# Kernel optimization log

Hardware: AMD Instinct MI355X
Metric: run time of the kernel (lower is better)

## Reference

```python
import jax, jax.numpy as jnp
import numpy as np

N_HEADS = 8

def setup_inputs() -> dict:
    key = jax.random.key(0)
    ks = jax.random.split(key, 7)
    B, S, D = 4, 2048, 512
    s = 1.0 / np.sqrt(D)
    return {
        "input_Q": jax.random.normal(ks[0], (B, S, D), jnp.float32),
        "input_K": jax.random.normal(ks[1], (B, S, D), jnp.float32),
        "input_V": jax.random.normal(ks[2], (B, S, D), jnp.float32),
        "W_Q": jax.random.normal(ks[3], (D, D), jnp.float32) * s,
        "W_K": jax.random.normal(ks[4], (D, D), jnp.float32) * s,
        "W_V": jax.random.normal(ks[5], (D, D), jnp.float32) * s,
        "W_O": jax.random.normal(ks[6], (D, D), jnp.float32) * s,
    }

def reference(input_Q, input_K, input_V, W_Q, W_K, W_V, W_O):
    B, Sq, D = input_Q.shape
    Sk = input_K.shape[1]
    H = N_HEADS
    d_k = D // H
    # torch nn.Linear(bias=False): y = x @ W.T
    def proj(x, W):
        return (x @ W.T).reshape(B, -1, H, d_k).transpose(0, 2, 1, 3)  # [B,H,S,dk]
    Q = proj(input_Q, W_Q)
    K = proj(input_K, W_K)
    V = proj(input_V, W_V)
    scale = 1.0 / jnp.sqrt(jnp.float32(d_k))
    scores = jnp.einsum("bhqd,bhkd->bhqk", Q, K) * scale  # [B,H,Sq,Sk]
    # TriangularCausalMask: mask strict upper triangle with -inf
    causal = jnp.tril(jnp.ones((Sq, Sk), dtype=bool))
    scores = jnp.where(causal[None, None], scores, -jnp.inf)
    attn = jax.nn.softmax(scores, axis=-1)
    context = jnp.einsum("bhqk,bhkd->bhqd", attn, V)
    context = context.transpose(0, 2, 1, 3).reshape(B, Sq, D)
    return context @ W_O.T
```

## Files before the change

### kernel.cpp

```cpp
#include <hip/hip_runtime.h>
#include <hip/hip_bf16.h>
#include <math.h>

#define B_  4
#define S_  2048
#define D_  512
#define H_  8
#define DK_ 64
#define M_  (B_ * S_)

using bf16   = __bf16;
using bf16x4 = __bf16 __attribute__((ext_vector_type(4)));
using bf16x8 = __bf16 __attribute__((ext_vector_type(8)));
using f32x4  = float __attribute__((ext_vector_type(4)));

#define MFMA16(a, b, c) __builtin_amdgcn_mfma_f32_16x16x32_bf16((a), (b), (c), 0, 0, 0)
#define EXP2(x) exp2f(x)

typedef __attribute__((address_space(3))) void       lds_void;
typedef const __attribute__((address_space(1))) void gbl_void;

__device__ __forceinline__ void async16(const bf16* g, bf16* lds) {
    __builtin_amdgcn_global_load_lds((gbl_void*)g, (lds_void*)lds, 16, 0, 0);
}

__device__ __forceinline__ bf16x8 ldg8(const bf16* p) {
    return *reinterpret_cast<const bf16x8*>(p);
}

__device__ __forceinline__ size_t fragbase(int g, int k0, int kk, int t) {
    return ((((size_t)(g * 8 + k0) * 2 + kk) * 4 + t) * 64) * 8;
}

__global__ __launch_bounds__(256) void cvt_all(
    const float* __restrict__ x0, const float* __restrict__ x1, const float* __restrict__ x2,
    const float* __restrict__ w0, const float* __restrict__ w1,
    const float* __restrict__ w2, const float* __restrict__ w3,
    bf16* __restrict__ dst)
{
    const size_t i = ((size_t)blockIdx.x * 256 + threadIdx.x) * 8;
    const float* src;
    size_t off, dbase;
    if (i < (size_t)3 << 22) {
        const int seg = (int)(i >> 22);
        off = i & (((size_t)1 << 22) - 1);
        src = (seg == 0) ? x0 : (seg == 1) ? x1 : x2;
        dbase = (size_t)seg << 22;
    } else {
        const size_t jj = i - ((size_t)3 << 22);
        const int seg = (int)(jj >> 18);
        off = jj & (((size_t)1 << 18) - 1);
        src = (seg == 0) ? w0 : (seg == 1) ? w1 : (seg == 2) ? w2 : w3;
        dbase = ((size_t)3 << 22) + ((size_t)seg << 18);
    }
    const int row = (int)(off >> 9), col = (int)(off & 511);
    const int g = row >> 6, t = (row >> 4) & 3, lc = row & 15;
    const int k0 = col >> 6, kk = (col >> 5) & 1, lg = (col >> 3) & 3;
    const size_t didx = dbase + fragbase(g, k0, kk, t) + (size_t)(lg * 16 + lc) * 8;

    f32x4 a = *reinterpret_cast<const f32x4*>(src + off);
    f32x4 b = *reinterpret_cast<const f32x4*>(src + off + 4);
    bf16x8 r;
    #pragma unroll
    for (int j = 0; j < 4; ++j) { r[j] = (bf16)a[j]; r[j + 4] = (bf16)b[j]; }
    *reinterpret_cast<bf16x8*>(dst + didx) = r;
}

__global__ __launch_bounds__(256) void gemm_qkv(
    const bf16* __restrict__ Xf, const bf16* __restrict__ Wf,
    bf16* __restrict__ qkv)
{
    const int bx  = blockIdx.x;
    const int xcd = bx & 7;
    const int idx = bx >> 3;
    const int mt  = xcd + 8 * (idx & 7);
    const int rest = idx >> 3;
    const int nt  = rest & 3;
    const int z   = rest >> 2;

    const bf16* Xz = Xf + (size_t)z * M_ * D_;
    const bf16* Wz = Wf + (size_t)z * D_ * D_;
    const bool vz = (z == 2);
    const bf16* A  = vz ? Xz : Wz;
    const bf16* Bm = vz ? Wz : Xz;

    const int lane = threadIdx.x & 63;
    const int wave = threadIdx.x >> 6;
    const int lc = lane & 15;
    const int lg = lane >> 4;
    const int gA = (vz ? 2 * mt : 2 * nt) + (wave >> 1);
    const int gB = (vz ? 2 * nt : 2 * mt) + (wave & 1);

    f32x4 acc[4][4] = {};

    #pragma unroll
    for (int k0 = 0; k0 < 8; ++k0) {
        #pragma unroll
        for (int kk = 0; kk < 2; ++kk) {
            bf16x8 af[4], bfm[4];
            #pragma unroll
            for (int t = 0; t < 4; ++t)
                af[t] = ldg8(A + fragbase(gA, k0, kk, t) + (size_t)lane * 8);
            #pragma unroll
            for (int t = 0; t < 4; ++t)
                bfm[t] = ldg8(Bm + fragbase(gB, k0, kk, t) + (size_t)lane * 8);
            #pragma unroll
            for (int mi = 0; mi < 4; ++mi)
                #pragma unroll
                for (int ni = 0; ni < 4; ++ni)
                    acc[mi][ni] = MFMA16(af[mi], bfm[ni], acc[mi][ni]);
        }
    }

    if (z < 2) {
        bf16* Y = qkv + (size_t)z * M_ * D_;
        const float sc = (z == 0) ? 0.125f * 1.4426950408889634f : 1.0f;
        #pragma unroll
        for (int mi = 0; mi < 4; ++mi)
            #pragma unroll
            for (int ni = 0; ni < 4; ++ni) {
                const int d = gA * 64 + mi * 16 + lg * 4;
                const int s = gB * 64 + ni * 16 + lc;
                bf16x4 v;
                #pragma unroll
                for (int r = 0; r < 4; ++r) v[r] = (bf16)(acc[mi][ni][r] * sc);
                const size_t oidx =
                    ((((size_t)(s >> 11) * H_ + (d >> 6)) * S_
                      + (s & (S_ - 1))) << 6) + (d & 63);
                *reinterpret_cast<bf16x4*>(&Y[oidx]) = v;
            }
    } else {
        bf16* Y = qkv + (size_t)2 * M_ * D_;
        #pragma unroll
        for (int mi = 0; mi < 4; ++mi)
            #pragma unroll
            for (int ni = 0; ni < 4; ++ni) {
                const int s = gA * 64 + mi * 16 + lg * 4;
                const int d = gB * 64 + ni * 16 + lc;
                bf16x4 v;
                #pragma unroll
                for (int r = 0; r < 4; ++r) v[r] = (bf16)acc[mi][ni][r];
                const size_t oidx =
                    ((((size_t)(s >> 11)) * H_ + (d >> 6)) << 17)
                    + (size_t)(d & 63) * S_ + (s & (S_ - 1));
                *reinterpret_cast<bf16x4*>(&Y[oidx]) = v;
            }
    }
}

__global__ __launch_bounds__(256) void gemm_out(
    const bf16* __restrict__ CtxF, const bf16* __restrict__ WoF,
    float* __restrict__ out)
{
    const int bx  = blockIdx.x;
    const int xcd = bx & 7;
    const int idx = bx >> 3;
    const int mt  = xcd + 8 * (idx & 15);
    const int nt  = idx >> 4;

    const int lane = threadIdx.x & 63;
    const int wave = threadIdx.x >> 6;
    const int lc = lane & 15;
    const int lg = lane >> 4;
    const int gA = 2 * nt + (wave >> 1);
    const int tA = (wave & 1) * 2;
    const int gB = mt;

    f32x4 acc[2][4] = {};

    #pragma unroll
    for (int k0 = 0; k0 < 8; ++k0) {
        #pragma unroll
        for (int kk = 0; kk < 2; ++kk) {
            bf16x8 af[2], bfm[4];
            #pragma unroll
            for (int ai = 0; ai < 2; ++ai)
                af[ai] = ldg8(WoF + fragbase(gA, k0, kk, tA + ai) + (size_t)lane * 8);
            #pragma unroll
            for (int t = 0; t < 4; ++t)
                bfm[t] = ldg8(CtxF + fragbase(gB, k0, kk, t) + (size_t)lane * 8);
            #pragma unroll
            for (int ai = 0; ai < 2; ++ai)
                #pragma unroll
                for (int ni = 0; ni < 4; ++ni)
                    acc[ai][ni] = MFMA16(af[ai], bfm[ni], acc[ai][ni]);
        }
    }

    #pragma unroll
    for (int ai = 0; ai < 2; ++ai)
        #pragma unroll
        for (int ni = 0; ni < 4; ++ni) {
            const int d = gA * 64 + (tA + ai) * 16 + lg * 4;
            const int s = gB * 64 + ni * 16 + lc;
            *reinterpret_cast<f32x4*>(&out[(size_t)s * D_ + d]) = acc[ai][ni];
        }
}

__global__ __launch_bounds__(256) void attn(
    const bf16* __restrict__ QKV, bf16* __restrict__ CtxF)
{
    const int bx = blockIdx.x;
    const int bh = (bx & 7) * 4 + ((bx >> 3) & 3);
    const int pi = bx >> 5;
    const int b = bh >> 3, h = bh & 7;
    const size_t plane = (size_t)S_ * DK_;
    const bf16* Q  = QKV + (size_t)bh * plane;
    const bf16* Kp = QKV + (size_t)(B_ * H_) * plane + (size_t)bh * plane;
    const bf16* Vt = QKV + 2 * (size_t)(B_ * H_) * plane + (size_t)bh * plane;

    const int lane = threadIdx.x & 63;
    const int wave = threadIdx.x >> 6;
    const int lc = lane & 15;
    const int lg = lane >> 4;
    const int srow = wave * 16 + lc;
    const int mrow = wave * 16 + lc;

    __shared__ bf16 Ks[2][64 * 64];
    __shared__ bf16 Vs[2][64 * 64];
    __shared__ bf16 Pw[4][1280];

    const int lo = pi;
    const int hi = 31 - pi;

    const int qL = lo * 64 + mrow;
    const int qH = hi * 64 + mrow;
    bf16x8 qfL0 = ldg8(Q + (size_t)qL * DK_ + lg * 8);
    bf16x8 qfL1 = ldg8(Q + (size_t)qL * DK_ + 32 + lg * 8);
    bf16x8 qfH0 = ldg8(Q + (size_t)qH * DK_ + lg * 8);
    bf16x8 qfH1 = ldg8(Q + (size_t)qH * DK_ + 32 + lg * 8);

    f32x4 accL[4] = {}, accH[4] = {};
    float liL = 0.f, liH = 0.f;

    #pragma unroll
    for (int i = 0; i < 2; ++i) {
        const int kc = i * 4 + lg;
        async16(Kp + (size_t)srow * DK_ + kc * 8, Ks[0] + (i * 256 + wave * 64) * 8);
        async16(Vt + (size_t)srow * S_ + kc * 8,  Vs[0] + (i * 256 + wave * 64) * 8);
    }

    for (int j = 0; j <= hi; ++j) {
        __syncthreads();
        if (j < hi) {
            const int kn = (j + 1) * 64;
            bf16* kd = Ks[(j + 1) & 1];
            bf16* vd = Vs[(j + 1) & 1];
            #pragma unroll
            for (int i = 0; i < 2; ++i) {
                const int kc = i * 4 + lg;
                async16(Kp + (size_t)(kn + srow) * DK_ + kc * 8,
                        kd + (i * 256 + wave * 64) * 8);
                async16(Vt + (size_t)srow * S_ + kn + kc * 8,
                        vd + (i * 256 + wave * 64) * 8);
            }
        }
        const bf16* ks = Ks[j & 1];
        const bf16* vs = Vs[j & 1];
        bf16* Pp = &Pw[wave][0];

        bf16x8 kf0[4], kf1[4], vf0[4], vf1[4];
        #pragma unroll
        for (int t = 0; t < 4; ++t) {
            kf0[t] = ldg8(&ks[(t * 64 + lane) * 8]);
            kf1[t] = ldg8(&ks[(256 + t * 64 + lane) * 8]);
            vf0[t] = ldg8(&vs[(t * 64 + lane) * 8]);
            vf1[t] = ldg8(&vs[(256 + t * 64 + lane) * 8]);
        }

        auto step = [&](const bf16x8& qf0, const bf16x8& qf1, bool diag,
                        f32x4* accO, float& li) {
            f32x4 st[4];
            #pragma unroll
            for (int t = 0; t < 4; ++t) {
                f32x4 zz = {};
                zz = MFMA16(kf0[t], qf0, zz);
                st[t] = MFMA16(kf1[t], qf1, zz);
            }
            float rs = 0.f;
            if (diag) {
                #pragma unroll
                for (int t = 0; t < 4; ++t)
                    #pragma unroll
                    for (int r = 0; r < 4; ++r) {
                        const int kl = t * 16 + lg * 4 + r;
                        const float pv = EXP2((kl <= mrow) ? st[t][r] : -1e30f);
                        st[t][r] = pv;
                        rs += pv;
                    }
            } else {
                #pragma unroll
                for (int t = 0; t < 4; ++t)
                    #pragma unroll
                    for (int r = 0; r < 4; ++r) {
                        const float pv = EXP2(st[t][r]);
                        st[t][r] = pv;
                        rs += pv;
                    }
            }
            li += rs;

            #pragma unroll
            for (int t = 0; t < 4; ++t) {
                bf16x4 pv;
                #pragma unroll
                for (int r = 0; r < 4; ++r) pv[r] = (bf16)st[t][r];
                *reinterpret_cast<bf16x4*>(
                    &Pp[((2 * t + (lg >> 1)) * 16 + lc) * 8 + (lg & 1) * 4]) = pv;
            }
            bf16x8 p0 = ldg8(&Pp[lane * 8]);
            bf16x8 p1 = ldg8(&Pp[(64 + lane) * 8]);

            #pragma unroll
            for (int t = 0; t < 4; ++t) {
                accO[t] = MFMA16(vf0[t], p0, accO[t]);
                accO[t] = MFMA16(vf1[t], p1, accO[t]);
            }
        };

        step(qfH0, qfH1, j == hi, accH, liH);
        if (j <= lo) step(qfL0, qfL1, j == lo, accL, liL);
    }

    liL += __shfl_xor(liL, 16); liL += __shfl_xor(liL, 32);
    liH += __shfl_xor(liH, 16); liH += __shfl_xor(liH, 32);
    const float rlL = 1.0f / liL;
    const float rlH = 1.0f / liH;
    bf16* T = &Pw[wave][0];

    #pragma unroll
    for (int half = 0; half < 2; ++half) {
        const f32x4* accO = half ? accH : accL;
        const float rl = half ? rlH : rlL;
        const int jq = half ? hi : lo;
        #pragma unroll
        for (int t = 0; t < 4; ++t) {
            bf16x4 ov;
            #pragma unroll
            for (int r = 0; r < 4; ++r) ov[r] = (bf16)(accO[t][r] * rl);
            *reinterpret_cast<bf16x4*>(&T[lc * 72 + t * 16 + lg * 4]) = ov;
        }
        #pragma unroll
        for (int kk = 0; kk < 2; ++kk) {
            bf16x8 o8 = ldg8(&T[lc * 72 + kk * 32 + lg * 8]);
            *reinterpret_cast<bf16x8*>(
                &CtxF[fragbase(b * 32 + jq, h, kk, wave) + (size_t)lane * 8]) = o8;
        }
    }
}

extern "C" void kernel_launch(void* const* d_in, const int* in_sizes, int n_in,
                              void* d_out, int out_size, void* d_ws, size_t ws_size,
                              hipStream_t stream)
{
    float* out = (float*)d_out;

    bf16* Xf   = (bf16*)d_ws;
    bf16* Wf   = Xf + (size_t)3 * M_ * D_;
    bf16* qkv  = Wf + (size_t)4 * D_ * D_;
    bf16* ctxF = qkv + (size_t)3 * M_ * D_;

    cvt_all<<<6656, 256, 0, stream>>>(
        (const float*)d_in[0], (const float*)d_in[1], (const float*)d_in[2],
        (const float*)d_in[3], (const float*)d_in[4], (const float*)d_in[5],
        (const float*)d_in[6], Xf);

    gemm_qkv<<<dim3(768), 256, 0, stream>>>(Xf, Wf, qkv);
    attn<<<dim3(512), 256, 0, stream>>>(qkv, ctxF);
    gemm_out<<<dim3(512), 256, 0, stream>>>(ctxF, Wf + (size_t)3 * D_ * D_, out);
}
```

Baseline: 188.7 us.

## Replace LDS P-matrix round trip with permlane16 swaps and remap V loads

In the attention kernel, the softmax probabilities are now repacked into MFMA B-operand fragments with permlane16_swap register exchanges instead of a write-to-LDS/read-back per step. The V tile's global-to-LDS column order is permuted to match the new register layout of P, and the per-wave P scratch buffer is dropped, with the epilogue reusing the K buffer after a barrier. The conversion kernel is also re-indexed so each wave writes a contiguous fragment block, reading strided source rows instead of scattering writes. This removes LDS traffic and waits from the inner loop, at the cost of relying on a newer cross-lane instruction and a correct permutation.

```diff
diff --git a/kernel.cpp b/kernel.cpp
--- a/kernel.cpp
+++ b/kernel.cpp
@@ -38,32 +38,32 @@
     const float* __restrict__ w2, const float* __restrict__ w3,
     bf16* __restrict__ dst)
 {
-    const size_t i = ((size_t)blockIdx.x * 256 + threadIdx.x) * 8;
+    const int w    = blockIdx.x * 4 + (threadIdx.x >> 6);
+    const int lane = threadIdx.x & 63;
+    const int lg = lane >> 4, lc = lane & 15;
     const float* src;
-    size_t off, dbase;
-    if (i < (size_t)3 << 22) {
-        const int seg = (int)(i >> 22);
-        off = i & (((size_t)1 << 22) - 1);
+    int c;
+    size_t dbase;
+    if (w < 24576) {
+        const int seg = w >> 13;
+        c = w & 8191;
         src = (seg == 0) ? x0 : (seg == 1) ? x1 : x2;
         dbase = (size_t)seg << 22;
     } else {
-        const size_t jj = i - ((size_t)3 << 22);
-        const int seg = (int)(jj >> 18);
-        off = jj & (((size_t)1 << 18) - 1);
+        const int jj = w - 24576;
+        const int seg = jj >> 9;
+        c = jj & 511;
         src = (seg == 0) ? w0 : (seg == 1) ? w1 : (seg == 2) ? w2 : w3;
         dbase = ((size_t)3 << 22) + ((size_t)seg << 18);
     }
-    const int row = (int)(off >> 9), col = (int)(off & 511);
-    const int g = row >> 6, t = (row >> 4) & 3, lc = row & 15;
-    const int k0 = col >> 6, kk = (col >> 5) & 1, lg = (col >> 3) & 3;
-    const size_t didx = dbase + fragbase(g, k0, kk, t) + (size_t)(lg * 16 + lc) * 8;
-
-    f32x4 a = *reinterpret_cast<const f32x4*>(src + off);
-    f32x4 b = *reinterpret_cast<const f32x4*>(src + off + 4);
+    const int g = c >> 6, k0 = (c >> 3) & 7, kk = (c >> 2) & 1, t = c & 3;
+    const size_t soff = ((size_t)(g * 64 + t * 16 + lc) << 9) + k0 * 64 + kk * 32 + lg * 8;
+    f32x4 a = *reinterpret_cast<const f32x4*>(src + soff);
+    f32x4 b = *reinterpret_cast<const f32x4*>(src + soff + 4);
     bf16x8 r;
     #pragma unroll
     for (int j = 0; j < 4; ++j) { r[j] = (bf16)a[j]; r[j + 4] = (bf16)b[j]; }
-    *reinterpret_cast<bf16x8*>(dst + didx) = r;
+    *reinterpret_cast<bf16x8*>(dst + dbase + ((size_t)c << 9) + (size_t)lane * 8) = r;
 }
 
 __global__ __launch_bounds__(256) void gemm_qkv(
@@ -195,6 +195,18 @@
             const int s = gB * 64 + ni * 16 + lc;
             *reinterpret_cast<f32x4*>(&out[(size_t)s * D_ + d]) = acc[ai][ni];
         }
+}
+
+__device__ __forceinline__ bf16x8 pfrag(const f32x4 a, const f32x4 b) {
+    union U4 { bf16x4 v; unsigned int u[2]; };
+    U4 pa, pb;
+    #pragma unroll
+    for (int r = 0; r < 4; ++r) { pa.v[r] = (bf16)a[r]; pb.v[r] = (bf16)b[r]; }
+    auto r0 = __builtin_amdgcn_permlane16_swap(pa.u[0], pb.u[0], false, false);
+    auto r1 = __builtin_amdgcn_permlane16_swap(pa.u[1], pb.u[1], false, false);
+    union U8 { unsigned int u[4]; bf16x8 v; } out;
+    out.u[0] = r0[0]; out.u[1] = r1[0]; out.u[2] = r0[1]; out.u[3] = r1[1];
+    return out.v;
 }
 
 __global__ __launch_bounds__(256) void attn(
@@ -213,12 +225,12 @@
     const int wave = threadIdx.x >> 6;
     const int lc = lane & 15;
     const int lg = lane >> 4;
+    const int sg = ((lg & 1) << 1) | (lg >> 1);
     const int srow = wave * 16 + lc;
     const int mrow = wave * 16 + lc;
 
     __shared__ bf16 Ks[2][64 * 64];
     __shared__ bf16 Vs[2][64 * 64];
-    __shared__ bf16 Pw[4][1280];
 
     const int lo = pi;
     const int hi = 31 - pi;
@@ -235,9 +247,10 @@
 
     #pragma unroll
     for (int i = 0; i < 2; ++i) {
-        const int kc = i * 4 + lg;
-        async16(Kp + (size_t)srow * DK_ + kc * 8, Ks[0] + (i * 256 + wave * 64) * 8);
-        async16(Vt + (size_t)srow * S_ + kc * 8,  Vs[0] + (i * 256 + wave * 64) * 8);
+        const int kc  = i * 4 + lg;
+        const int kcv = i * 4 + sg;
+        async16(Kp + (size_t)srow * DK_ + kc * 8,  Ks[0] + (i * 256 + wave * 64) * 8);
+        async16(Vt + (size_t)srow * S_  + kcv * 8, Vs[0] + (i * 256 + wave * 64) * 8);
     }
 
     for (int j = 0; j <= hi; ++j) {
@@ -248,16 +261,16 @@
             bf16* vd = Vs[(j + 1) & 1];
             #pragma unroll
             for (int i = 0; i < 2; ++i) {
-                const int kc = i * 4 + lg;
+                const int kc  = i * 4 + lg;
+                const int kcv = i * 4 + sg;
                 async16(Kp + (size_t)(kn + srow) * DK_ + kc * 8,
                         kd + (i * 256 + wave * 64) * 8);
-                async16(Vt + (size_t)srow * S_ + kn + kc * 8,
+                async16(Vt + (size_t)srow * S_ + kn + kcv * 8,
                         vd + (i * 256 + wave * 64) * 8);
             }
         }
         const bf16* ks = Ks[j & 1];
         const bf16* vs = Vs[j & 1];
-        bf16* Pp = &Pw[wave][0];
 
         bf16x8 kf0[4], kf1[4], vf0[4], vf1[4];
         #pragma unroll
@@ -300,16 +313,8 @@
             }
             li += rs;
 
-            #pragma unroll
-            for (int t = 0; t < 4; ++t) {
-                bf16x4 pv;
-                #pragma unroll
-                for (int r = 0; r < 4; ++r) pv[r] = (bf16)st[t][r];
-                *reinterpret_cast<bf16x4*>(
-                    &Pp[((2 * t + (lg >> 1)) * 16 + lc) * 8 + (lg & 1) * 4]) = pv;
-            }
-            bf16x8 p0 = ldg8(&Pp[lane * 8]);
-            bf16x8 p1 = ldg8(&Pp[(64 + lane) * 8]);
+            const bf16x8 p0 = pfrag(st[0], st[1]);
+            const bf16x8 p1 = pfrag(st[2], st[3]);
 
             #pragma unroll
             for (int t = 0; t < 4; ++t) {
@@ -326,7 +331,8 @@
     liH += __shfl_xor(liH, 16); liH += __shfl_xor(liH, 32);
     const float rlL = 1.0f / liL;
     const float rlH = 1.0f / liH;
-    bf16* T = &Pw[wave][0];
+    __syncthreads();
+    bf16* T = &Ks[0][0] + wave * 1280;
 
     #pragma unroll
     for (int half = 0; half < 2; ++half) {
```

Result: faster. 182.5 us (-3.2%).
